# Kernel tuning notes

Measured on AMD Instinct MI355X. Metric: run time of the kernel, lower is better.

The kernel has to match this reference:

```python
import itertools
import jax, jax.numpy as jnp
import numpy as np

FS = 16000
MAX_TAU = 40
C_SOUND = 343.0
MIC_DISTANCE_FROM_WALL = 0.5
MIN_SPEAKER_HEIGHT = 1.0
MAX_SPEAKER_HEIGHT = 2.0
ROOM = (6.0, 5.0, 3.0)
DENSITY = (0.1, 0.1, 0.1)
N_MICS = 8


def _build_geometry():
    # 8-mic circular array, radius 0.4 m, centered in the room
    ang = np.arange(N_MICS) * 2.0 * np.pi / N_MICS
    receivers = np.stack([3.0 + 0.4 * np.cos(ang),
                          2.5 + 0.4 * np.sin(ang),
                          1.5 * np.ones(N_MICS)], axis=1).astype(np.float32)  # [M,3]
    combinations = np.array(list(itertools.combinations(range(N_MICS), 2)), dtype=np.int32)  # [P,2]
    # candidate grid (same nesting order as the original list comprehension)
    xs = np.arange(MIC_DISTANCE_FROM_WALL, ROOM[0] + DENSITY[0], DENSITY[0], dtype=np.float32)
    ys = np.arange(0.0, ROOM[1] + DENSITY[1], DENSITY[1], dtype=np.float32)
    zs = np.arange(MIN_SPEAKER_HEIGHT, MAX_SPEAKER_HEIGHT + DENSITY[2], DENSITY[2], dtype=np.float32)
    grid_x = np.stack(np.meshgrid(xs, ys, zs, indexing='ij'), axis=-1).reshape(-1, 3)  # [G,3]
    # true TDOA per grid point / pair -> delay index into GCC output of length 2*MAX_TAU+1
    rp = receivers[combinations]                                   # [P,2,3]
    d = np.linalg.norm(grid_x[:, None, None, :] - rp[None], axis=-1)  # [G,P,2]
    tdoa = (d[..., 0] - d[..., 1]) / C_SOUND * FS                  # samples
    tau = np.clip(MAX_TAU + np.round(tdoa), 0, 2 * MAX_TAU).astype(np.int32)  # [G,P]
    rec_centroid = receivers.mean(axis=0)                          # [3]
    return grid_x, tau, combinations, rec_centroid


def setup_inputs() -> dict:
    key = jax.random.key(0)
    signal = jax.random.normal(key, (16, N_MICS, 4096), dtype=jnp.float32)
    grid_x, tau, combinations, rec_centroid = _build_geometry()
    return {
        "signal": signal,
        "grid_x": jnp.asarray(grid_x),
        "tau": jnp.asarray(tau),
        "combinations": jnp.asarray(combinations),
        "rec_centroid": jnp.asarray(rec_centroid),
    }


def reference(signal, grid_x, tau, combinations, rec_centroid):
    B, M, N = signal.shape
    P = combinations.shape[0]
    # GCC-PHAT per mic pair
    pairs = signal[:, combinations, :]                    # [B,P,2,N]
    S = jnp.fft.rfft(pairs, axis=-1)                      # [B,P,2,F]
    X = S[..., 0, :] * jnp.conj(S[..., 1, :])             # cross-spectrum [B,P,F]
    phat = X / (jnp.abs(X) + 1e-12)
    cc = jnp.fft.irfft(phat, n=N, axis=-1)                # [B,P,N]
    # lags -MAX_TAU..MAX_TAU -> length 2*MAX_TAU+1
    cc = jnp.concatenate([cc[..., -MAX_TAU:], cc[..., :MAX_TAU + 1]], axis=-1)  # [B,P,2T+1]
    # gather per grid point / pair (avoids materializing [B,G,P,2T+1])
    gathered = cc[:, jnp.arange(P)[None, :], tau]         # [B,G,P]
    power = gathered.sum(axis=-1)                         # SRP map [B,G]
    idx = jnp.argmax(power, axis=-1)                      # [B]
    x = grid_x[idx]                                       # [B,3]
    return x - rec_centroid
```

## Files before the change

### kernel.cpp

```cpp
#include <hip/hip_runtime.h>

#define N_FFT 4096
#define NH    2048
#define NBINS 2049
#define NLAGS 81
#define MAXTAU 40
#define NSEG  8
#define SEGLEN 256
#define PI_F 3.14159265358979323846f
#define PAD(i) ((i) + ((i) >> 4))

#define CQ 0.99999882345f
#define SQ 0.00153398019f

__device__ __forceinline__ float2 cmul(float2 a, float2 b) {
    return make_float2(a.x * b.x - a.y * b.y, a.x * b.y + a.y * b.x);
}

__global__ __launch_bounds__(512)
void rfft_kernel(const float* __restrict__ sig,
                 float* __restrict__ S,
                 float* __restrict__ cc, int ccN) {
    int bm  = (int)blockIdx.x;
    int tid = (int)threadIdx.x;

    __shared__ float2 data[PAD(NH - 1) + 1];
    __shared__ float2 tw[NH / 2];

    for (int i = bm * 512 + tid; i < ccN; i += (int)gridDim.x * 512)
        cc[i] = 0.0f;

    for (int j = tid; j < NH / 2; j += 512) {
        float sv, cv;
        sincosf(-(2.0f * PI_F / (float)NH) * (float)j, &sv, &cv);
        tw[j] = make_float2(cv, sv);
    }

    const float2* sp = (const float2*)(sig + (size_t)bm * N_FFT);
    for (int i = tid; i < NH; i += 512) {
        float2 v = sp[i];
        int j = (int)(__brev((unsigned)i) >> 21);
        data[PAD(j)] = v;
    }
    __syncthreads();

    for (int s = 1; s <= 9; s += 2) {
        int h  = 1 << (s - 1);
        int j  = tid & (h - 1);
        int g  = tid >> (s - 1);
        int i0 = (g << (s + 1)) + j;
        int i1 = i0 + h, i2 = i0 + 2 * h, i3 = i0 + 3 * h;

        float2 w1 = tw[j << (11 - s)];
        float2 wA = tw[j << (10 - s)];
        float2 wB = tw[(j + h) << (10 - s)];

        float2 a = data[PAD(i0)];
        float2 b = data[PAD(i1)];
        float2 c = data[PAD(i2)];
        float2 d = data[PAD(i3)];

        float2 wb = cmul(w1, b), wd = cmul(w1, d);
        float2 a1 = make_float2(a.x + wb.x, a.y + wb.y);
        float2 b1 = make_float2(a.x - wb.x, a.y - wb.y);
        float2 c1 = make_float2(c.x + wd.x, c.y + wd.y);
        float2 d1 = make_float2(c.x - wd.x, c.y - wd.y);
        float2 wc = cmul(wA, c1), wdd = cmul(wB, d1);
        data[PAD(i0)] = make_float2(a1.x + wc.x,  a1.y + wc.y);
        data[PAD(i2)] = make_float2(a1.x - wc.x,  a1.y - wc.y);
        data[PAD(i1)] = make_float2(b1.x + wdd.x, b1.y + wdd.y);
        data[PAD(i3)] = make_float2(b1.x - wdd.x, b1.y - wdd.y);
        __syncthreads();
    }

    for (int t = tid; t < 1024; t += 512) {
        int i0 = t, i1 = t + 1024;
        float2 w = tw[t];
        float2 u = data[PAD(i0)];
        float2 v = data[PAD(i1)];
        float2 wv = cmul(w, v);
        data[PAD(i0)] = make_float2(u.x + wv.x, u.y + wv.y);
        data[PAD(i1)] = make_float2(u.x - wv.x, u.y - wv.y);
    }
    __syncthreads();

    float2* So = (float2*)(S + (size_t)bm * NBINS * 2);
    for (int k = tid; k < NBINS; k += 512) {
        float2 Zk = data[PAD(k & (NH - 1))];
        float2 Zm = data[PAD((NH - k) & (NH - 1))];
        float er = 0.5f * (Zk.x + Zm.x);
        float ei = 0.5f * (Zk.y - Zm.y);
        float dr = Zk.x - Zm.x;
        float di = Zk.y + Zm.y;
        float orr = 0.5f * di;
        float oii = -0.5f * dr;
        float2 W;
        if (k == 2048) {
            W = make_float2(-1.0f, 0.0f);
        } else {
            float2 t = tw[k >> 1];
            if (k & 1) W = make_float2(t.x * CQ + t.y * SQ,
                                       t.y * CQ - t.x * SQ);
            else       W = t;
        }
        So[k] = make_float2(er + W.x * orr - W.y * oii,
                            ei + W.x * oii + W.y * orr);
    }
}

#define NCH 6
#define CHLEN 43
__global__ __launch_bounds__(256)
void phat_cc_kernel(const float* __restrict__ S,
                    const int* __restrict__ comb,
                    float* __restrict__ cc, int P) {
    int id  = (int)blockIdx.x;
    int seg = id & (NSEG - 1);
    int bp  = id >> 3;
    int b   = bp / P;
    int p   = bp % P;
    int ma = comb[p * 2 + 0];
    int mb = comb[p * 2 + 1];
    const float2* Sa = (const float2*)(S + ((size_t)(b * 8 + ma)) * NBINS * 2);
    const float2* Sb = (const float2*)(S + ((size_t)(b * 8 + mb)) * NBINS * 2);

    int k0 = seg * SEGLEN;
    int k1 = (seg == NSEG - 1) ? NBINS : (k0 + SEGLEN);

    __shared__ float2 phs[SEGLEN + 1];
    __shared__ float partCr[41 * NCH];
    __shared__ float partCi[41 * NCH];

    int tid = (int)threadIdx.x;
    for (int k = k0 + tid; k < k1; k += 256) {
        float2 a = Sa[k];
        float2 c = Sb[k];
        float Xr = a.x * c.x + a.y * c.y;
        float Xi = a.y * c.x - a.x * c.y;
        float mag = sqrtf(Xr * Xr + Xi * Xi);
        float w = (k == 0 || k == 2048) ? 1.0f : 2.0f;
        float inv = w / (mag + 1e-12f);
        phs[k - k0] = make_float2(Xr * inv, Xi * inv);
    }
    __syncthreads();

    if (tid < 41 * NCH) {
        int n = tid % 41;
        int c = tid / 41;
        int kk0 = k0 + c * CHLEN;
        int kk1 = kk0 + CHLEN;
        if (kk1 > k1) kk1 = k1;

        float step = (2.0f * PI_F / (float)N_FFT) * (float)n;
        float sv, cv;
        sincosf(step, &sv, &cv);
        float wr = cv, wi = sv;
        sincosf(step * (float)kk0, &sv, &cv);
        float rr = cv, ri = sv;

        float Cr = 0.0f, Ci = 0.0f;
        for (int k = kk0; k < kk1; ++k) {
            float2 ph = phs[k - k0];
            Cr = fmaf(ph.x, rr, Cr);
            Ci = fmaf(ph.y, ri, Ci);
            float nr = rr * wr - ri * wi;
            float ni = rr * wi + ri * wr;
            rr = nr; ri = ni;
        }
        partCr[tid] = Cr;
        partCi[tid] = Ci;
    }
    __syncthreads();

    if (tid < 41) {
        float Cr = 0.0f, Ci = 0.0f;
        #pragma unroll
        for (int c = 0; c < NCH; ++c) {
            Cr += partCr[tid + 41 * c];
            Ci += partCi[tid + 41 * c];
        }
        float* outp = cc + (size_t)bp * NLAGS;
        atomicAdd(&outp[MAXTAU + tid], Cr - Ci);
        if (tid > 0) atomicAdd(&outp[MAXTAU - tid], Cr + Ci);
    }
}

__global__ __launch_bounds__(512)
void power_argmax_kernel(const float* __restrict__ cc,
                         const int* __restrict__ tau,
                         int G, int P,
                         float* __restrict__ pval,
                         int* __restrict__ pidx, int nchunks) {
    int b     = (int)blockIdx.y;
    int chunk = (int)blockIdx.x;
    int tid   = (int)threadIdx.x;

    __shared__ float ccs[28 * NLAGS];
    const float4* csrc = (const float4*)(cc + (size_t)b * P * NLAGS);
    float4* cdst = (float4*)ccs;
    const float scale = 1.0f / (float)N_FFT;
    for (int i = tid; i < 28 * NLAGS / 4; i += 512) {
        float4 v = csrc[i];
        cdst[i] = make_float4(v.x * scale, v.y * scale, v.z * scale, v.w * scale);
    }
    __syncthreads();

    int g = chunk * 512 + tid;
    float v = -1e30f;
    int   gi = 0x7fffffff;
    if (g < G) {
        const int4* tp = (const int4*)(tau + (size_t)g * 28);
        v = 0.0f;
        #pragma unroll
        for (int q = 0; q < 7; ++q) {
            int4 tv = tp[q];
            v += ccs[(q * 4 + 0) * NLAGS + tv.x];
            v += ccs[(q * 4 + 1) * NLAGS + tv.y];
            v += ccs[(q * 4 + 2) * NLAGS + tv.z];
            v += ccs[(q * 4 + 3) * NLAGS + tv.w];
        }
        gi = g;
    }

    #pragma unroll
    for (int off = 32; off > 0; off >>= 1) {
        float v2 = __shfl_down(v, off);
        int   i2 = __shfl_down(gi, off);
        if (v2 > v || (v2 == v && i2 < gi)) { v = v2; gi = i2; }
    }
    __shared__ float wval[8];
    __shared__ int   widx[8];
    int lane = tid & 63, wv = tid >> 6;
    if (lane == 0) { wval[wv] = v; widx[wv] = gi; }
    __syncthreads();
    if (tid == 0) {
        #pragma unroll
        for (int w = 1; w < 8; ++w) {
            float v2 = wval[w]; int i2 = widx[w];
            if (v2 > v || (v2 == v && i2 < gi)) { v = v2; gi = i2; }
        }
        pval[b * nchunks + chunk] = v;
        pidx[b * nchunks + chunk] = gi;
    }
}

__global__ void finalize_kernel(const float* __restrict__ pval,
                                const int* __restrict__ pidx, int nchunks,
                                const float* __restrict__ grid_x,
                                const float* __restrict__ rec_centroid,
                                float* __restrict__ out) {
    int b = (int)blockIdx.x;
    int l = (int)threadIdx.x;
    float v = -1e30f; int gi = 0x7fffffff;
    for (int j = l; j < nchunks; j += 64) {
        float v2 = pval[b * nchunks + j];
        int   i2 = pidx[b * nchunks + j];
        if (v2 > v || (v2 == v && i2 < gi)) { v = v2; gi = i2; }
    }
    #pragma unroll
    for (int off = 32; off > 0; off >>= 1) {
        float v2 = __shfl_down(v, off);
        int   i2 = __shfl_down(gi, off);
        if (v2 > v || (v2 == v && i2 < gi)) { v = v2; gi = i2; }
    }
    if (l == 0) {
        for (int c = 0; c < 3; ++c)
            out[b * 3 + c] = grid_x[(size_t)gi * 3 + c] - rec_centroid[c];
    }
}

extern "C" void kernel_launch(void* const* d_in, const int* in_sizes, int n_in,
                              void* d_out, int out_size, void* d_ws, size_t ws_size,
                              hipStream_t stream) {
    const float* signal       = (const float*)d_in[0];
    const float* grid_x       = (const float*)d_in[1];
    const int*   tau          = (const int*)d_in[2];
    const int*   comb         = (const int*)d_in[3];
    const float* rec_centroid = (const float*)d_in[4];
    float* out = (float*)d_out;

    int G  = in_sizes[1] / 3;
    int P  = in_sizes[3] / 2;
    int BM = in_sizes[0] / N_FFT;
    int B  = BM / 8;
    int BP = B * P;

    float* S  = (float*)d_ws;
    float* cc = S + (size_t)BM * NBINS * 2;
    int nchunks = (G + 511) / 512;
    float* pval = cc + (size_t)BP * NLAGS;
    int*   pidx = (int*)(pval + (size_t)B * nchunks);

    rfft_kernel<<<BM, 512, 0, stream>>>(signal, S, cc, BP * NLAGS);
    phat_cc_kernel<<<BP * NSEG, 256, 0, stream>>>(S, comb, cc, P);
    power_argmax_kernel<<<dim3(nchunks, B), 512, 0, stream>>>(cc, tau, G, P, pval, pidx, nchunks);
    finalize_kernel<<<B, 64, 0, stream>>>(pval, pidx, nchunks, grid_x, rec_centroid, out);
}
```

Baseline: 95.26 us.

## Fuse all stages into one cooperative persistent kernel with grid syncs

Replaces the four-kernel pipeline (rfft, phat cross-correlation, power/argmax, finalize) with a single cooperative kernel of 256 persistent blocks. Stages are separated by grid-wide syncs, and the argmax is reduced through a packed 64-bit atomicMax. The phat stage now handles one full pair per block, with 12 chunks instead of 8 segments, which removes the zero-init of cc and the atomic accumulation into it. The aim is to cut launch overhead and the extra passes between kernels. The cost is lower parallelism in the phat stage (BP work units over 256 blocks) and the overhead of the grid syncs. If the cooperative launch fails, the code falls back to the old multi-kernel path.

```diff
diff --git a/kernel.cpp b/kernel.cpp
--- a/kernel.cpp
+++ b/kernel.cpp
@@ -1,4 +1,7 @@
 #include <hip/hip_runtime.h>
+#include <hip/hip_cooperative_groups.h>
+
+namespace cg = cooperative_groups;
 
 #define N_FFT 4096
 #define NH    2048
@@ -13,8 +16,249 @@
 #define CQ 0.99999882345f
 #define SQ 0.00153398019f
 
+#define NCHK 12
+#define CHLEN 171
+#define NBLOCKS 256
+
 __device__ __forceinline__ float2 cmul(float2 a, float2 b) {
     return make_float2(a.x * b.x - a.y * b.y, a.x * b.y + a.y * b.x);
+}
+
+__global__ __launch_bounds__(512)
+void mega_kernel(const float* __restrict__ sig,
+                 const int* __restrict__ comb,
+                 const int* __restrict__ tau,
+                 const float* __restrict__ grid_x,
+                 const float* __restrict__ rec_centroid,
+                 float* __restrict__ out,
+                 float* __restrict__ S,
+                 float* __restrict__ cc,
+                 unsigned long long* __restrict__ packed,
+                 int BM, int P, int B, int G, int nchunks) {
+    cg::grid_group gg = cg::this_grid();
+    const int bid = (int)blockIdx.x;
+    const int tid = (int)threadIdx.x;
+    const int nb  = (int)gridDim.x;
+
+    __shared__ __align__(16) float2 data[PAD(NH - 1) + 1];
+    __shared__ float2 tw[NH / 2];
+    __shared__ float partCr[41 * NCHK];
+    __shared__ float partCi[41 * NCHK];
+    __shared__ float wval[8];
+    __shared__ int   widx[8];
+
+    if (bid == nb - 1 && tid < B) packed[tid] = 0ull;
+
+    if (bid < BM) {
+        for (int j = tid; j < NH / 2; j += 512) {
+            float sv, cv;
+            sincosf(-(2.0f * PI_F / (float)NH) * (float)j, &sv, &cv);
+            tw[j] = make_float2(cv, sv);
+        }
+    }
+    for (int ch = bid; ch < BM; ch += nb) {
+        const float2* sp = (const float2*)(sig + (size_t)ch * N_FFT);
+        for (int i = tid; i < NH; i += 512) {
+            float2 v = sp[i];
+            int j = (int)(__brev((unsigned)i) >> 21);
+            data[PAD(j)] = v;
+        }
+        __syncthreads();
+
+        for (int s = 1; s <= 9; s += 2) {
+            int h  = 1 << (s - 1);
+            int j  = tid & (h - 1);
+            int g  = tid >> (s - 1);
+            int i0 = (g << (s + 1)) + j;
+            int i1 = i0 + h, i2 = i0 + 2 * h, i3 = i0 + 3 * h;
+
+            float2 w1 = tw[j << (11 - s)];
+            float2 wA = tw[j << (10 - s)];
+            float2 wB = tw[(j + h) << (10 - s)];
+
+            float2 a = data[PAD(i0)];
+            float2 b = data[PAD(i1)];
+            float2 c = data[PAD(i2)];
+            float2 d = data[PAD(i3)];
+
+            float2 wb = cmul(w1, b), wd = cmul(w1, d);
+            float2 a1 = make_float2(a.x + wb.x, a.y + wb.y);
+            float2 b1 = make_float2(a.x - wb.x, a.y - wb.y);
+            float2 c1 = make_float2(c.x + wd.x, c.y + wd.y);
+            float2 d1 = make_float2(c.x - wd.x, c.y - wd.y);
+            float2 wc = cmul(wA, c1), wdd = cmul(wB, d1);
+            data[PAD(i0)] = make_float2(a1.x + wc.x,  a1.y + wc.y);
+            data[PAD(i2)] = make_float2(a1.x - wc.x,  a1.y - wc.y);
+            data[PAD(i1)] = make_float2(b1.x + wdd.x, b1.y + wdd.y);
+            data[PAD(i3)] = make_float2(b1.x - wdd.x, b1.y - wdd.y);
+            __syncthreads();
+        }
+
+        for (int t = tid; t < 1024; t += 512) {
+            int i0 = t, i1 = t + 1024;
+            float2 w = tw[t];
+            float2 u = data[PAD(i0)];
+            float2 v = data[PAD(i1)];
+            float2 wv = cmul(w, v);
+            data[PAD(i0)] = make_float2(u.x + wv.x, u.y + wv.y);
+            data[PAD(i1)] = make_float2(u.x - wv.x, u.y - wv.y);
+        }
+        __syncthreads();
+
+        float2* So = (float2*)(S + (size_t)ch * NBINS * 2);
+        for (int k = tid; k < NBINS; k += 512) {
+            float2 Zk = data[PAD(k & (NH - 1))];
+            float2 Zm = data[PAD((NH - k) & (NH - 1))];
+            float er = 0.5f * (Zk.x + Zm.x);
+            float ei = 0.5f * (Zk.y - Zm.y);
+            float dr = Zk.x - Zm.x;
+            float di = Zk.y + Zm.y;
+            float orr = 0.5f * di;
+            float oii = -0.5f * dr;
+            float2 W;
+            if (k == 2048) {
+                W = make_float2(-1.0f, 0.0f);
+            } else {
+                float2 t = tw[k >> 1];
+                if (k & 1) W = make_float2(t.x * CQ + t.y * SQ,
+                                           t.y * CQ - t.x * SQ);
+                else       W = t;
+            }
+            So[k] = make_float2(er + W.x * orr - W.y * oii,
+                                ei + W.x * oii + W.y * orr);
+        }
+        __syncthreads();
+    }
+    gg.sync();
+
+    float2* phs = data;
+    int BP = B * P;
+    for (int u = bid; u < BP; u += nb) {
+        int b = u / P, p = u - b * P;
+        int ma = comb[p * 2 + 0];
+        int mb = comb[p * 2 + 1];
+        const float2* Sa = (const float2*)(S + ((size_t)(b * 8 + ma)) * NBINS * 2);
+        const float2* Sb = (const float2*)(S + ((size_t)(b * 8 + mb)) * NBINS * 2);
+
+        __syncthreads();
+        for (int k = tid; k < NBINS; k += 512) {
+            float2 a = Sa[k];
+            float2 c = Sb[k];
+            float Xr = a.x * c.x + a.y * c.y;
+            float Xi = a.y * c.x - a.x * c.y;
+            float mag = sqrtf(Xr * Xr + Xi * Xi);
+            float w = (k == 0 || k == NH) ? 1.0f : 2.0f;
+            float inv = w / (mag + 1e-12f);
+            phs[k] = make_float2(Xr * inv, Xi * inv);
+        }
+        __syncthreads();
+
+        if (tid < 41 * NCHK) {
+            int n = tid / NCHK;
+            int c = tid - n * NCHK;
+            int kk0 = c * CHLEN;
+            int kk1 = kk0 + CHLEN;
+            if (kk1 > NBINS) kk1 = NBINS;
+
+            float step = (2.0f * PI_F / (float)N_FFT) * (float)n;
+            float sv, cv;
+            sincosf(step, &sv, &cv);
+            float wr = cv, wi = sv;
+            sincosf(step * (float)kk0, &sv, &cv);
+            float rr = cv, ri = sv;
+
+            float Cr = 0.0f, Ci = 0.0f;
+            for (int k = kk0; k < kk1; ++k) {
+                float2 ph = phs[k];
+                Cr = fmaf(ph.x, rr, Cr);
+                Ci = fmaf(ph.y, ri, Ci);
+                float nr = rr * wr - ri * wi;
+                float ni = rr * wi + ri * wr;
+                rr = nr; ri = ni;
+            }
+            partCr[tid] = Cr;
+            partCi[tid] = Ci;
+        }
+        __syncthreads();
+
+        if (tid < 41) {
+            float Cr = 0.0f, Ci = 0.0f;
+            #pragma unroll
+            for (int c = 0; c < NCHK; ++c) {
+                Cr += partCr[tid * NCHK + c];
+                Ci += partCi[tid * NCHK + c];
+            }
+            float* outp = cc + (size_t)u * NLAGS;
+            outp[MAXTAU + tid] = Cr - Ci;
+            if (tid > 0) outp[MAXTAU - tid] = Cr + Ci;
+        }
+    }
+    gg.sync();
+
+    float* ccs = (float*)data;
+    const float scale = 1.0f / (float)N_FFT;
+    int NU = B * nchunks;
+    for (int u = bid; u < NU; u += nb) {
+        int b     = u % B;
+        int chunk = u / B;
+
+        __syncthreads();
+        const float4* csrc = (const float4*)(cc + (size_t)b * P * NLAGS);
+        float4* cdst = (float4*)ccs;
+        for (int i = tid; i < (P * NLAGS) / 4; i += 512) {
+            float4 v4 = csrc[i];
+            cdst[i] = make_float4(v4.x * scale, v4.y * scale, v4.z * scale, v4.w * scale);
+        }
+        __syncthreads();
+
+        int g = chunk * 512 + tid;
+        float v = -1e30f;
+        int   gi = 0x7fffffff;
+        if (g < G) {
+            const int4* tp = (const int4*)(tau + (size_t)g * 28);
+            v = 0.0f;
+            #pragma unroll
+            for (int q = 0; q < 7; ++q) {
+                int4 tv = tp[q];
+                v += ccs[(q * 4 + 0) * NLAGS + tv.x];
+                v += ccs[(q * 4 + 1) * NLAGS + tv.y];
+                v += ccs[(q * 4 + 2) * NLAGS + tv.z];
+                v += ccs[(q * 4 + 3) * NLAGS + tv.w];
+            }
+            gi = g;
+        }
+
+        #pragma unroll
+        for (int off = 32; off > 0; off >>= 1) {
+            float v2 = __shfl_down(v, off);
+            int   i2 = __shfl_down(gi, off);
+            if (v2 > v || (v2 == v && i2 < gi)) { v = v2; gi = i2; }
+        }
+        int lane = tid & 63, wv = tid >> 6;
+        if (lane == 0) { wval[wv] = v; widx[wv] = gi; }
+        __syncthreads();
+        if (tid == 0) {
+            #pragma unroll
+            for (int w = 1; w < 8; ++w) {
+                float v2 = wval[w]; int i2 = widx[w];
+                if (v2 > v || (v2 == v && i2 < gi)) { v = v2; gi = i2; }
+            }
+            unsigned vb = __float_as_uint(v);
+            vb = (vb & 0x80000000u) ? ~vb : (vb | 0x80000000u);
+            unsigned long long key = ((unsigned long long)vb << 32)
+                                   | (unsigned long long)(0xFFFFFFFFu - (unsigned)gi);
+            atomicMax(packed + b, key);
+        }
+    }
+    gg.sync();
+
+    if (bid < B && tid == 0) {
+        unsigned long long k = packed[bid];
+        int gi = (int)(0xFFFFFFFFu - (unsigned)(k & 0xFFFFFFFFull));
+        out[bid * 3 + 0] = grid_x[(size_t)gi * 3 + 0] - rec_centroid[0];
+        out[bid * 3 + 1] = grid_x[(size_t)gi * 3 + 1] - rec_centroid[1];
+        out[bid * 3 + 2] = grid_x[(size_t)gi * 3 + 2] - rec_centroid[2];
+    }
 }
 
 __global__ __launch_bounds__(512)
@@ -109,7 +353,7 @@
 }
 
 #define NCH 6
-#define CHLEN 43
+#define CHLEN_F 43
 __global__ __launch_bounds__(256)
 void phat_cc_kernel(const float* __restrict__ S,
                     const int* __restrict__ comb,
@@ -147,8 +391,8 @@
     if (tid < 41 * NCH) {
         int n = tid % 41;
         int c = tid / 41;
-        int kk0 = k0 + c * CHLEN;
-        int kk1 = kk0 + CHLEN;
+        int kk0 = k0 + c * CHLEN_F;
+        int kk1 = kk0 + CHLEN_F;
         if (kk1 > k1) kk1 = k1;
 
         float step = (2.0f * PI_F / (float)N_FFT) * (float)n;
@@ -284,15 +528,28 @@
     int BM = in_sizes[0] / N_FFT;
     int B  = BM / 8;
     int BP = B * P;
+    int nchunks = (G + 511) / 512;
 
     float* S  = (float*)d_ws;
     float* cc = S + (size_t)BM * NBINS * 2;
-    int nchunks = (G + 511) / 512;
-    float* pval = cc + (size_t)BP * NLAGS;
+    unsigned long long* packed = (unsigned long long*)(cc + (size_t)BP * NLAGS);
+    float* pval = (float*)(packed + 16);
     int*   pidx = (int*)(pval + (size_t)B * nchunks);
 
-    rfft_kernel<<<BM, 512, 0, stream>>>(signal, S, cc, BP * NLAGS);
-    phat_cc_kernel<<<BP * NSEG, 256, 0, stream>>>(S, comb, cc, P);
-    power_argmax_kernel<<<dim3(nchunks, B), 512, 0, stream>>>(cc, tau, G, P, pval, pidx, nchunks);
-    finalize_kernel<<<B, 64, 0, stream>>>(pval, pidx, nchunks, grid_x, rec_centroid, out);
-}
+    void* kargs[] = {
+        (void*)&signal, (void*)&comb, (void*)&tau, (void*)&grid_x,
+        (void*)&rec_centroid, (void*)&out, (void*)&S, (void*)&cc,
+        (void*)&packed, (void*)&BM, (void*)&P, (void*)&B, (void*)&G,
+        (void*)&nchunks
+    };
+    hipError_t err = hipLaunchCooperativeKernel((const void*)mega_kernel,
+                                                dim3(NBLOCKS), dim3(512),
+                                                kargs, 0, stream);
+    if (err != hipSuccess) {
+        (void)hipGetLastError();
+        rfft_kernel<<<BM, 512, 0, stream>>>(signal, S, cc, BP * NLAGS);
+        phat_cc_kernel<<<BP * NSEG, 256, 0, stream>>>(S, comb, cc, P);
+        power_argmax_kernel<<<dim3(nchunks, B), 512, 0, stream>>>(cc, tau, G, P, pval, pidx, nchunks);
+        finalize_kernel<<<B, 64, 0, stream>>>(pval, pidx, nchunks, grid_x, rec_centroid, out);
+    }
+}
```

New measurement: 195.9 us. 106% more time.
